# Performance work log

Hardware: AMD Instinct MI355X
Metric: run time of the kernel (lower is better)

## Reference

```python
import jax, jax.numpy as jnp
import numpy as np

B = 32768
Z_DIM = 64
X_DIM = 256
HIDDEN = 512
T = 8            # num_transforms
NBINS = 8
TAIL = 25.0
MULT = 3 * NBINS - 1   # widths + heights + interior derivatives = 23
MIN_W = 1e-3
MIN_H = 1e-3
MIN_D = 1e-3


def _masks():
    # MADE degrees (nflows, random_mask=False)
    d_in = np.arange(1, Z_DIM + 1)                      # input degrees 1..D
    h = np.arange(HIDDEN) % (Z_DIM - 1) + 1             # hidden degrees
    o = np.arange(Z_DIM * MULT) // MULT + 1             # output degrees, MULT contiguous per feature
    m1 = (h[:, None] >= d_in[None, :]).astype(np.float32)   # [H, D]
    m2 = (h[:, None] >= h[None, :]).astype(np.float32)      # [H, H]
    m3 = (o[:, None] > h[None, :]).astype(np.float32)       # [D*MULT, H] strict for output layer
    return jnp.asarray(m1), jnp.asarray(m2), jnp.asarray(m3)


def _rq_spline_fwd(z, uw, uh, ud):
    """Unconstrained rational-quadratic spline with linear tails (forward).
    z: [B, D]; uw/uh: [B, D, NBINS]; ud: [B, D, NBINS-1].
    Returns (outputs [B,D], logabsdet [B,D])."""
    const = np.log(np.exp(1.0 - MIN_D) - 1.0)
    pad = jnp.full(ud.shape[:-1] + (1,), const, ud.dtype)
    ud = jnp.concatenate([pad, ud, pad], axis=-1)       # [B, D, NBINS+1]

    widths = jax.nn.softmax(uw, axis=-1)
    widths = MIN_W + (1.0 - MIN_W * NBINS) * widths
    zero = jnp.zeros(widths.shape[:-1] + (1,), widths.dtype)
    cumw = jnp.concatenate([zero, jnp.cumsum(widths, axis=-1)], axis=-1)
    cumw = -TAIL + 2.0 * TAIL * cumw
    cumw = cumw.at[..., 0].set(-TAIL).at[..., -1].set(TAIL)
    widths = cumw[..., 1:] - cumw[..., :-1]

    derivs = MIN_D + jax.nn.softplus(ud)

    heights = jax.nn.softmax(uh, axis=-1)
    heights = MIN_H + (1.0 - MIN_H * NBINS) * heights
    cumh = jnp.concatenate([zero, jnp.cumsum(heights, axis=-1)], axis=-1)
    cumh = -TAIL + 2.0 * TAIL * cumh
    cumh = cumh.at[..., 0].set(-TAIL).at[..., -1].set(TAIL)
    heights = cumh[..., 1:] - cumh[..., :-1]

    delta = heights / widths

    z_in = jnp.clip(z, -TAIL, TAIL)
    edges = cumw.at[..., -1].add(1e-6)                  # nflows searchsorted eps
    idx = jnp.sum(z_in[..., None] >= edges, axis=-1) - 1
    idx = jnp.clip(idx, 0, NBINS - 1)

    g = lambda a: jnp.take_along_axis(a, idx[..., None], axis=-1)[..., 0]
    in_cw = g(cumw); in_w = g(widths)
    in_ch = g(cumh); in_h = g(heights)
    in_dl = g(delta)
    d0 = g(derivs); d1 = g(derivs[..., 1:])

    th = (z_in - in_cw) / in_w
    th1 = th * (1.0 - th)
    num = in_h * (in_dl * th * th + d0 * th1)
    den = in_dl + (d0 + d1 - 2.0 * in_dl) * th1
    out = in_ch + num / den
    dnum = in_dl ** 2 * (d1 * th * th + 2.0 * in_dl * th1 + d0 * (1.0 - th) ** 2)
    lad = jnp.log(dnum) - 2.0 * jnp.log(den)

    inside = (z >= -TAIL) & (z <= TAIL)
    return jnp.where(inside, out, z), jnp.where(inside, lad, 0.0)


def setup_inputs() -> dict:
    key = jax.random.key(0)
    ks = jax.random.split(key, 10)
    s = 0.05  # small init scale keeps spline params in a sane regime
    return {
        "z": jax.random.normal(ks[0], (B, Z_DIM), jnp.float32),
        "x": jax.random.normal(ks[1], (B, X_DIM), jnp.float32),
        "W1": jax.random.normal(ks[2], (T, HIDDEN, Z_DIM), jnp.float32) * s,
        "b1": jax.random.normal(ks[3], (T, HIDDEN), jnp.float32) * s,
        "Wc": jax.random.normal(ks[4], (T, HIDDEN, X_DIM), jnp.float32) * s,
        "bc": jax.random.normal(ks[5], (T, HIDDEN), jnp.float32) * s,
        "W2": jax.random.normal(ks[6], (T, HIDDEN, HIDDEN), jnp.float32) * s,
        "b2": jax.random.normal(ks[7], (T, HIDDEN), jnp.float32) * s,
        "W3": jax.random.normal(ks[8], (T, Z_DIM * MULT, HIDDEN), jnp.float32) * s,
        "b3": jax.random.normal(ks[9], (T, Z_DIM * MULT), jnp.float32) * s,
    }


def reference(z, x, W1, b1, Wc, bc, W2, b2, W3, b3):
    """log q(z|x) of the composed MADE-RQ-spline flow, shape [B]."""
    m1, m2, m3 = _masks()
    inv_sqrt_h = 1.0 / np.sqrt(HIDDEN)
    cur = z
    total_lad = jnp.zeros(z.shape[0], z.dtype)
    for t in range(T):
        # MADE: masked initial layer + context layer, one masked feedforward block (linear->relu), masked output layer
        h = cur @ (W1[t] * m1).T + b1[t] + x @ Wc[t].T + bc[t]
        h = jax.nn.relu(h @ (W2[t] * m2).T + b2[t])
        p = (h @ (W3[t] * m3).T + b3[t]).reshape(-1, Z_DIM, MULT)
        uw = p[..., :NBINS] * inv_sqrt_h
        uh = p[..., NBINS:2 * NBINS] * inv_sqrt_h
        ud = p[..., 2 * NBINS:]
        cur, lad = _rq_spline_fwd(cur, uw, uh, ud)
        total_lad = total_lad + lad.sum(axis=-1)
    log_base = -0.5 * jnp.sum(cur ** 2, axis=-1) - 0.5 * Z_DIM * np.log(2.0 * np.pi)
    return log_base + total_lad
```

## Files before the change

kernel.cpp:

```cpp
#include <hip/hip_runtime.h>
#include <cstdint>
#include <cstddef>

#define B_ROWS 32768
#define ZD 64
#define XD 256
#define HID 512
#define T_STEPS 8
#define MULT 23
#define MPAD 24
#define NOUT 1472
#define NPAD 1536
#define K1 320
#define PSTRIDE 200

typedef float f32x4 __attribute__((ext_vector_type(4)));
typedef short s16x8 __attribute__((ext_vector_type(8)));

__device__ __forceinline__ unsigned short f2bf(float f) {
  unsigned int u = __float_as_uint(f);
  u = (u + 0x7FFFu + ((u >> 16) & 1u)) >> 16;
  return (unsigned short)u;
}
__device__ __forceinline__ float bf2f(unsigned short s) {
  return __uint_as_float(((unsigned int)s) << 16);
}

__device__ __forceinline__ int permP(int n) {
  return (n < 72) ? (n / 9) + 63 * (n % 9)
                  : ((n - 72) >> 3) + 8 + 63 * ((n - 72) & 7);
}
__device__ __forceinline__ int degP(int n) {
  return (n < 72) ? (n / 9) + 1 : ((n - 72) >> 3) + 9;
}


__global__ void prep_w1cat(const float* __restrict__ W1, const float* __restrict__ Wc,
                           unsigned short* __restrict__ o) {
  int i = blockIdx.x * 256 + threadIdx.x;
  if (i >= T_STEPS * HID * K1) return;
  int t = i / (HID * K1);
  int r = i - t * (HID * K1);
  int n = r / K1;
  int k = r - n * K1;
  int on = permP(n);
  float v;
  if (k < ZD) {
    v = ((on % 63) >= k) ? W1[((size_t)t * HID + on) * ZD + k] : 0.0f;
  } else {
    v = Wc[((size_t)t * HID + on) * XD + (k - ZD)];
  }
  o[i] = f2bf(v);
}

__global__ void prep_w2(const float* __restrict__ W2, unsigned short* __restrict__ o) {
  int i = blockIdx.x * 256 + threadIdx.x;
  if (i >= T_STEPS * HID * HID) return;
  int t = i / (HID * HID);
  int r = i - t * (HID * HID);
  int n = r / HID;
  int k = r - n * HID;
  float v = 0.0f;
  if (degP(n) >= degP(k))
    v = W2[((size_t)t * HID + permP(n)) * HID + permP(k)];
  o[i] = f2bf(v);
}

__global__ void prep_w3(const float* __restrict__ W3, unsigned short* __restrict__ o) {
  int i = blockIdx.x * 256 + threadIdx.x;
  if (i >= T_STEPS * NPAD * HID) return;
  int t = i / (NPAD * HID);
  int r = i - t * (NPAD * HID);
  int n = r / HID;
  int k = r - n * HID;
  int d = n / MPAD;
  int jj = n - d * MPAD;
  float v = 0.0f;
  if (jj < MULT && d >= degP(k))
    v = W3[((size_t)t * NOUT + d * MULT + jj) * HID + permP(k)];
  o[i] = f2bf(v);
}

__global__ void prep_bias(const float* __restrict__ b1, const float* __restrict__ bc,
                          const float* __restrict__ b2, const float* __restrict__ b3,
                          float* __restrict__ ob1, float* __restrict__ ob2,
                          float* __restrict__ ob3) {
  int i = blockIdx.x * 256 + threadIdx.x;
  if (i < T_STEPS * HID) {
    int t = i / HID, n = i - t * HID;
    int on = permP(n);
    ob1[i] = b1[(size_t)t * HID + on] + bc[(size_t)t * HID + on];
  } else if (i < 2 * T_STEPS * HID) {
    int j = i - T_STEPS * HID;
    int t = j / HID, n = j - t * HID;
    ob2[j] = b2[(size_t)t * HID + permP(n)];
  } else {
    int j = i - 2 * T_STEPS * HID;
    if (j < T_STEPS * NPAD) {
      int t = j / NPAD;
      int n = j - t * NPAD;
      int d = n / MPAD;
      int jj = n - d * MPAD;
      ob3[j] = (jj < MULT) ? b3[(size_t)t * NOUT + d * MULT + jj] : 0.0f;
    }
  }
}

__global__ void prep_x(const float* __restrict__ x, unsigned short* __restrict__ A1) {
  int i = blockIdx.x * 256 + threadIdx.x;
  if (i >= B_ROWS * XD) return;
  int b = i >> 8;
  int j = i & 255;
  A1[(size_t)b * K1 + ZD + j] = f2bf(x[i]);
}

__global__ void prep_init(const float* __restrict__ z, unsigned short* __restrict__ A1,
                          float* __restrict__ curf, float* __restrict__ lad) {
  int i = blockIdx.x * 256 + threadIdx.x;
  if (i >= B_ROWS * ZD) return;
  int b = i >> 6;
  int d = i & 63;
  float zv = z[i];
  A1[(size_t)b * K1 + d] = f2bf(zv);
  curf[i] = zv;
  if (d == 0) lad[b] = 0.0f;
}


#define ASYNC16(gp, lp) __builtin_amdgcn_global_load_lds( \
    (__attribute__((address_space(1))) unsigned int*)(gp), \
    (__attribute__((address_space(3))) unsigned int*)(lp), 16, 0, 0)


__global__ __launch_bounds__(256, 2) void gemm_bias(
    const unsigned short* __restrict__ A,
    const unsigned short* __restrict__ Bw,
    const float* __restrict__ bias,
    unsigned short* __restrict__ C,
    int M, int N, int K, int relu, int tri)
{
  __shared__ alignas(16) unsigned short lA[128 * 32];
  __shared__ alignas(16) unsigned short lB[128 * 32];

  const int tid  = threadIdx.x;
  const int lane = tid & 63;
  const int wave = tid >> 6;

  const int lin = blockIdx.y * 4 + blockIdx.x;
  const int xcd = lin & 7;
  const int loc = lin >> 3;
  const int m0 = (xcd * 32 + (loc >> 2)) * 128;
  const int n0 = (loc & 3) * 128;
  const int Keff = tri ? min(K, 192 + n0) : K;

  const int wm = (wave >> 1) * 64;
  const int wn = (wave & 1) * 64;

  const int f    = tid * 16;
  const int row0 = f >> 6;
  const int colb = f & 63;

  char* gA0 = (char*)A  + ((size_t)(m0 + row0) * K) * 2 + colb;
  char* gA1 = gA0 + (size_t)64 * K * 2;
  char* gB0 = (char*)Bw + ((size_t)(n0 + row0) * K) * 2 + colb;
  char* gB1 = gB0 + (size_t)64 * K * 2;

  unsigned short* lA0 = lA + wave * 512;
  unsigned short* lA1 = lA + 2048 + wave * 512;
  unsigned short* lB0 = lB + wave * 512;
  unsigned short* lB1 = lB + 2048 + wave * 512;

  f32x4 acc[4][4];
#pragma unroll
  for (int i = 0; i < 4; i++)
#pragma unroll
    for (int j = 0; j < 4; j++) acc[i][j] = (f32x4){0.f, 0.f, 0.f, 0.f};

  const int fr  = lane & 15;
  const int fkb = (lane >> 4) * 16;
  const char* lab = (const char*)lA;
  const char* lbb = (const char*)lB;

  for (int k0 = 0; k0 < Keff; k0 += 32) {
    ASYNC16(gA0, lA0);
    ASYNC16(gA1, lA1);
    ASYNC16(gB0, lB0);
    ASYNC16(gB1, lB1);
    gA0 += 64; gA1 += 64; gB0 += 64; gB1 += 64;
    __syncthreads();

    s16x8 af[4], bfr[4];
#pragma unroll
    for (int i = 0; i < 4; i++)
      af[i] = *(const s16x8*)(lab + (wm + i * 16 + fr) * 64 + fkb);
#pragma unroll
    for (int i = 0; i < 4; i++)
      bfr[i] = *(const s16x8*)(lbb + (wn + i * 16 + fr) * 64 + fkb);

#pragma unroll
    for (int i = 0; i < 4; i++)
#pragma unroll
      for (int j = 0; j < 4; j++)
        acc[i][j] = __builtin_amdgcn_mfma_f32_16x16x32_bf16(af[i], bfr[j], acc[i][j], 0, 0, 0);
    __syncthreads();
  }

#pragma unroll
  for (int j = 0; j < 4; j++) {
    const int col = n0 + wn + j * 16 + fr;
    const float bv = bias[col];
#pragma unroll
    for (int i = 0; i < 4; i++) {
      const int rbase = m0 + wm + i * 16 + (lane >> 4) * 4;
#pragma unroll
      for (int r = 0; r < 4; r++) {
        float v = acc[i][j][r] + bv;
        if (relu) v = fmaxf(v, 0.0f);
        C[(size_t)(rbase + r) * N + col] = f2bf(v);
      }
    }
  }
}


__device__ __forceinline__ void rq_spline(const unsigned short* __restrict__ pp,
                                          float zv, float& zn, float& lad) {
  const float TAILC = 25.0f;
  const float MIN_WC = 0.001f;
  const float MIN_DC = 0.001f;
  const float SCALE = 0.044194173824159216f;

  s16x8 vw = *(const s16x8*)(pp);
  s16x8 vh = *(const s16x8*)(pp + 8);
  s16x8 vd = *(const s16x8*)(pp + 16);

  bool inside = (zv >= -TAILC) && (zv <= TAILC);
  float z_in = fminf(fmaxf(zv, -TAILC), TAILC);

  float ew[8], eh[8], sw = 0.f, sh = 0.f;
#pragma unroll
  for (int i = 0; i < 8; i++) {
    float u = fminf(fmaxf(bf2f((unsigned short)vw[i]) * SCALE, -30.f), 30.f);
    ew[i] = __expf(u); sw += ew[i];
  }
#pragma unroll
  for (int i = 0; i < 8; i++) {
    float u = fminf(fmaxf(bf2f((unsigned short)vh[i]) * SCALE, -30.f), 30.f);
    eh[i] = __expf(u); sh += eh[i];
  }
  float iw = (1.0f - 8.0f * MIN_WC) / sw;
  float ih = (1.0f - 8.0f * MIN_WC) / sh;

  float cumw[9], cumh[9];
  cumw[0] = -TAILC; cumh[0] = -TAILC;
  float cw = 0.f, ch = 0.f;
#pragma unroll
  for (int i = 0; i < 8; i++) {
    cw += MIN_WC + ew[i] * iw;
    ch += MIN_WC + eh[i] * ih;
    cumw[i + 1] = fmaf(2.0f * TAILC, cw, -TAILC);
    cumh[i + 1] = fmaf(2.0f * TAILC, ch, -TAILC);
  }
  cumw[8] = TAILC; cumh[8] = TAILC;

  int idx = 0;
#pragma unroll
  for (int i = 1; i < 8; i++) idx += (z_in >= cumw[i]) ? 1 : 0;

  float in_cw = 0.f, cw1 = 1.f, in_ch = 0.f, ch1 = 1.f, u0 = 0.f, u1 = 0.f;
#pragma unroll
  for (int i = 0; i < 8; i++) {
    if (i == idx) {
      in_cw = cumw[i]; cw1 = cumw[i + 1];
      in_ch = cumh[i]; ch1 = cumh[i + 1];
      u0 = (i > 0) ? bf2f((unsigned short)vd[i - 1]) : 0.0f;
      u1 = (i < 7) ? bf2f((unsigned short)vd[i]) : 0.0f;
    }
  }
  float dd0 = (idx == 0) ? 1.0f
            : MIN_DC + fmaxf(u0, 0.f) + __logf(1.0f + __expf(-fabsf(u0)));
  float dd1 = (idx == 7) ? 1.0f
            : MIN_DC + fmaxf(u1, 0.f) + __logf(1.0f + __expf(-fabsf(u1)));
  float in_w = cw1 - in_cw;
  float in_h = ch1 - in_ch;

  float delta = in_h / in_w;
  float th  = (z_in - in_cw) / in_w;
  float th1 = th * (1.0f - th);
  float th2 = th * th;
  float num = in_h * (delta * th2 + dd0 * th1);
  float den = delta + (dd0 + dd1 - 2.0f * delta) * th1;
  float outz = in_ch + num / den;
  float omt = 1.0f - th;
  float dnum = delta * delta * (dd1 * th2 + 2.0f * delta * th1 + dd0 * omt * omt);
  float l = __logf(dnum) - 2.0f * __logf(den);

  zn  = inside ? outz : zv;
  lad = inside ? l : 0.0f;
}


__global__ __launch_bounds__(256, 3) void gemm3_spline(
    const unsigned short* __restrict__ A,
    const unsigned short* __restrict__ Bw,
    const float* __restrict__ bias,
    float* __restrict__ curf,
    unsigned short* __restrict__ A1,
    float* __restrict__ lad_acc)
{
  __shared__ alignas(16) union {
    struct { unsigned short A[128 * 32]; unsigned short B[192 * 32]; } g;
    unsigned short p[128 * PSTRIDE];
  } sm;

  const int tid  = threadIdx.x;
  const int lane = tid & 63;
  const int wave = tid >> 6;

  const int lin = blockIdx.y * 8 + blockIdx.x;
  const int xcd = lin & 7;
  const int loc = lin >> 3;
  const int m0 = (xcd * 32 + (loc >> 3)) * 128;
  const int bn = loc & 7;
  const int n0 = bn * 192;
  const int Keff = 64 * (bn + 1);

  const int wm = (wave >> 1) * 64;
  const int wn = (wave & 1) * 96;
  const int fr = lane & 15;

  const int srow = tid >> 1;
  const int sb = m0 + srow;
  const int dl0 = (tid & 1) * 4;
  const int d0 = bn * 8 + dl0;
  float4 cz = *(const float4*)(curf + (size_t)sb * ZD + d0);
  float bv[6];
#pragma unroll
  for (int j = 0; j < 6; j++) bv[j] = bias[n0 + wn + j * 16 + fr];

  const int f    = tid * 16;
  const int row0 = f >> 6;
  const int colb = f & 63;
  const int K = HID;

  char* gA0 = (char*)A  + ((size_t)(m0 + row0) * K) * 2 + colb;
  char* gA1 = gA0 + (size_t)64 * K * 2;
  char* gB0 = (char*)Bw + ((size_t)(n0 + row0) * K) * 2 + colb;
  char* gB1 = gB0 + (size_t)64 * K * 2;
  char* gB2 = gB1 + (size_t)64 * K * 2;

  unsigned short* lA0 = sm.g.A + wave * 512;
  unsigned short* lA1 = sm.g.A + 2048 + wave * 512;
  unsigned short* lB0 = sm.g.B + wave * 512;
  unsigned short* lB1 = sm.g.B + 2048 + wave * 512;
  unsigned short* lB2 = sm.g.B + 4096 + wave * 512;

  f32x4 acc[4][6];
#pragma unroll
  for (int i = 0; i < 4; i++)
#pragma unroll
    for (int j = 0; j < 6; j++) acc[i][j] = (f32x4){0.f, 0.f, 0.f, 0.f};

  const int fkb = (lane >> 4) * 16;
  const char* lab = (const char*)sm.g.A;
  const char* lbb = (const char*)sm.g.B;

  for (int k0 = 0; k0 < Keff; k0 += 32) {
    ASYNC16(gA0, lA0);
    ASYNC16(gA1, lA1);
    ASYNC16(gB0, lB0);
    ASYNC16(gB1, lB1);
    ASYNC16(gB2, lB2);
    gA0 += 64; gA1 += 64; gB0 += 64; gB1 += 64; gB2 += 64;
    __syncthreads();

    s16x8 af[4], bfr[6];
#pragma unroll
    for (int i = 0; i < 4; i++)
      af[i] = *(const s16x8*)(lab + (wm + i * 16 + fr) * 64 + fkb);
#pragma unroll
    for (int j = 0; j < 6; j++)
      bfr[j] = *(const s16x8*)(lbb + (wn + j * 16 + fr) * 64 + fkb);

#pragma unroll
    for (int i = 0; i < 4; i++)
#pragma unroll
      for (int j = 0; j < 6; j++)
        acc[i][j] = __builtin_amdgcn_mfma_f32_16x16x32_bf16(af[i], bfr[j], acc[i][j], 0, 0, 0);
    __syncthreads();
  }

#pragma unroll
  for (int j = 0; j < 6; j++) {
    const int col = wn + j * 16 + fr;
#pragma unroll
    for (int i = 0; i < 4; i++) {
      const int rbase = wm + i * 16 + (lane >> 4) * 4;
#pragma unroll
      for (int r = 0; r < 4; r++)
        sm.p[(rbase + r) * PSTRIDE + col] = f2bf(acc[i][j][r] + bv[j]);
    }
  }
  __syncthreads();

  const unsigned short* pp = sm.p + srow * PSTRIDE + dl0 * MPAD;
  float zn0, zn1, zn2, zn3, l0, l1, l2, l3;
  rq_spline(pp,            cz.x, zn0, l0);
  rq_spline(pp + MPAD,     cz.y, zn1, l1);
  rq_spline(pp + 2 * MPAD, cz.z, zn2, l2);
  rq_spline(pp + 3 * MPAD, cz.w, zn3, l3);

  *(float4*)(curf + (size_t)sb * ZD + d0) = make_float4(zn0, zn1, zn2, zn3);
  union { unsigned int u[2]; unsigned short s[4]; } pk;
  pk.s[0] = f2bf(zn0); pk.s[1] = f2bf(zn1); pk.s[2] = f2bf(zn2); pk.s[3] = f2bf(zn3);
  *(uint2*)(A1 + (size_t)sb * K1 + d0) = make_uint2(pk.u[0], pk.u[1]);

  float s = l0 + l1 + l2 + l3;
  s += __shfl_xor(s, 1, 64);
  if ((tid & 1) == 0) atomicAdd(&lad_acc[sb], s);
}


__global__ void finalize(const float* __restrict__ curf, const float* __restrict__ lad,
                         float* __restrict__ out) {
  int i = blockIdx.x * 256 + threadIdx.x;
  int b = i >> 6;
  int d = i & 63;
  float c = curf[i];
  float q = c * c;
#pragma unroll
  for (int off = 32; off > 0; off >>= 1) q += __shfl_xor(q, off, 64);
  if (d == 0) out[b] = lad[b] - 0.5f * q - 58.81206612509905f;
}


extern "C" void kernel_launch(void* const* d_in, const int* in_sizes, int n_in,
                              void* d_out, int out_size, void* d_ws, size_t ws_size,
                              hipStream_t stream)
{
  const float* z  = (const float*)d_in[0];
  const float* x  = (const float*)d_in[1];
  const float* W1 = (const float*)d_in[2];
  const float* b1 = (const float*)d_in[3];
  const float* Wc = (const float*)d_in[4];
  const float* bc = (const float*)d_in[5];
  const float* W2 = (const float*)d_in[6];
  const float* b2 = (const float*)d_in[7];
  const float* W3 = (const float*)d_in[8];
  const float* b3 = (const float*)d_in[9];
  float* out = (float*)d_out;
  char* ws = (char*)d_ws;

  size_t oA1 = 0;
  size_t oH1 = oA1 + (size_t)B_ROWS * K1 * 2;
  size_t oH2 = oH1 + (size_t)B_ROWS * HID * 2;
  size_t oCU = oH2 + (size_t)B_ROWS * HID * 2;
  size_t oLA = oCU + (size_t)B_ROWS * ZD * 4;
  size_t oW1 = oLA + (size_t)B_ROWS * 4;
  size_t oW2 = oW1 + (size_t)T_STEPS * HID * K1 * 2;
  size_t oW3 = oW2 + (size_t)T_STEPS * HID * HID * 2;
  size_t oB1 = oW3 + (size_t)T_STEPS * NPAD * HID * 2;
  size_t oB2 = oB1 + (size_t)T_STEPS * HID * 4;
  size_t oB3 = oB2 + (size_t)T_STEPS * HID * 4;

  unsigned short* A1  = (unsigned short*)(ws + oA1);
  unsigned short* h1  = (unsigned short*)(ws + oH1);
  unsigned short* h2  = (unsigned short*)(ws + oH2);
  float* curf = (float*)(ws + oCU);
  float* lad  = (float*)(ws + oLA);
  unsigned short* w1c = (unsigned short*)(ws + oW1);
  unsigned short* w2c = (unsigned short*)(ws + oW2);
  unsigned short* w3c = (unsigned short*)(ws + oW3);
  float* b1c = (float*)(ws + oB1);
  float* b2p = (float*)(ws + oB2);
  float* b3c = (float*)(ws + oB3);

  prep_w1cat<<<T_STEPS * HID * K1 / 256, 256, 0, stream>>>(W1, Wc, w1c);
  prep_w2<<<T_STEPS * HID * HID / 256, 256, 0, stream>>>(W2, w2c);
  prep_w3<<<T_STEPS * NPAD * HID / 256, 256, 0, stream>>>(W3, w3c);
  prep_bias<<<T_STEPS * (2 * HID + NPAD) / 256, 256, 0, stream>>>(
      b1, bc, b2, b3, b1c, b2p, b3c);
  prep_x<<<B_ROWS * XD / 256, 256, 0, stream>>>(x, A1);
  prep_init<<<B_ROWS * ZD / 256, 256, 0, stream>>>(z, A1, curf, lad);

  for (int t = 0; t < T_STEPS; ++t) {
    gemm_bias<<<dim3(4, B_ROWS / 128), 256, 0, stream>>>(
        A1, w1c + (size_t)t * HID * K1, b1c + (size_t)t * HID, h1,
        B_ROWS, HID, K1, 0, 0);
    gemm_bias<<<dim3(4, B_ROWS / 128), 256, 0, stream>>>(
        h1, w2c + (size_t)t * HID * HID, b2p + (size_t)t * HID, h2,
        B_ROWS, HID, HID, 1, 1);
    gemm3_spline<<<dim3(8, B_ROWS / 128), 256, 0, stream>>>(
        h2, w3c + (size_t)t * NPAD * HID, b3c + (size_t)t * NPAD,
        curf, A1, lad);
  }
  finalize<<<B_ROWS * ZD / 256, 256, 0, stream>>>(curf, lad, out);
}
```

Before: 998.5 us.

## Load GEMM operands directly from global into registers, bypassing LDS staging

Both GEMM kernels stop staging A/B tiles in shared memory through async global-to-LDS loads and barriers. Each wave now loads its MFMA fragments straight from global memory into registers, and gemm_bias double-buffers them in registers to hide latency. The spline kernel's thread-to-row mapping is changed and its shuffle reduction is replaced by one atomic per thread, and its launch bounds drop to 2 blocks per CU. This removes LDS traffic and syncs, but each wave now reloads shared tiles from L2 without cross-wave reuse, loads become 16-byte strided rows, and register pressure rises.

```diff
diff --git a/kernel.cpp b/kernel.cpp
--- a/kernel.cpp
+++ b/kernel.cpp
@@ -127,11 +127,6 @@
 }
 
 
-#define ASYNC16(gp, lp) __builtin_amdgcn_global_load_lds( \
-    (__attribute__((address_space(1))) unsigned int*)(gp), \
-    (__attribute__((address_space(3))) unsigned int*)(lp), 16, 0, 0)
-
-
 __global__ __launch_bounds__(256, 2) void gemm_bias(
     const unsigned short* __restrict__ A,
     const unsigned short* __restrict__ Bw,
@@ -139,9 +134,6 @@
     unsigned short* __restrict__ C,
     int M, int N, int K, int relu, int tri)
 {
-  __shared__ alignas(16) unsigned short lA[128 * 32];
-  __shared__ alignas(16) unsigned short lB[128 * 32];
-
   const int tid  = threadIdx.x;
   const int lane = tid & 63;
   const int wave = tid >> 6;
@@ -155,20 +147,17 @@
 
   const int wm = (wave >> 1) * 64;
   const int wn = (wave & 1) * 64;
-
-  const int f    = tid * 16;
-  const int row0 = f >> 6;
-  const int colb = f & 63;
-
-  char* gA0 = (char*)A  + ((size_t)(m0 + row0) * K) * 2 + colb;
-  char* gA1 = gA0 + (size_t)64 * K * 2;
-  char* gB0 = (char*)Bw + ((size_t)(n0 + row0) * K) * 2 + colb;
-  char* gB1 = gB0 + (size_t)64 * K * 2;
-
-  unsigned short* lA0 = lA + wave * 512;
-  unsigned short* lA1 = lA + 2048 + wave * 512;
-  unsigned short* lB0 = lB + wave * 512;
-  unsigned short* lB1 = lB + 2048 + wave * 512;
+  const int fr = lane & 15;
+  const int fk = (lane >> 4) * 8;
+
+  const unsigned short* ap[4];
+  const unsigned short* bp[4];
+#pragma unroll
+  for (int i = 0; i < 4; i++)
+    ap[i] = A + (size_t)(m0 + wm + i * 16 + fr) * K + fk;
+#pragma unroll
+  for (int j = 0; j < 4; j++)
+    bp[j] = Bw + (size_t)(n0 + wn + j * 16 + fr) * K + fk;
 
   f32x4 acc[4][4];
 #pragma unroll
@@ -176,34 +165,33 @@
 #pragma unroll
     for (int j = 0; j < 4; j++) acc[i][j] = (f32x4){0.f, 0.f, 0.f, 0.f};
 
-  const int fr  = lane & 15;
-  const int fkb = (lane >> 4) * 16;
-  const char* lab = (const char*)lA;
-  const char* lbb = (const char*)lB;
-
-  for (int k0 = 0; k0 < Keff; k0 += 32) {
-    ASYNC16(gA0, lA0);
-    ASYNC16(gA1, lA1);
-    ASYNC16(gB0, lB0);
-    ASYNC16(gB1, lB1);
-    gA0 += 64; gA1 += 64; gB0 += 64; gB1 += 64;
-    __syncthreads();
-
-    s16x8 af[4], bfr[4];
+  s16x8 a[4], b[4], an[4], bn[4];
+#pragma unroll
+  for (int i = 0; i < 4; i++) a[i] = *(const s16x8*)(ap[i]);
+#pragma unroll
+  for (int j = 0; j < 4; j++) b[j] = *(const s16x8*)(bp[j]);
+
+#pragma unroll 2
+  for (int k0 = 32; k0 < Keff; k0 += 32) {
+#pragma unroll
+    for (int i = 0; i < 4; i++) an[i] = *(const s16x8*)(ap[i] + k0);
+#pragma unroll
+    for (int j = 0; j < 4; j++) bn[j] = *(const s16x8*)(bp[j] + k0);
 #pragma unroll
     for (int i = 0; i < 4; i++)
-      af[i] = *(const s16x8*)(lab + (wm + i * 16 + fr) * 64 + fkb);
-#pragma unroll
-    for (int i = 0; i < 4; i++)
-      bfr[i] = *(const s16x8*)(lbb + (wn + i * 16 + fr) * 64 + fkb);
-
-#pragma unroll
-    for (int i = 0; i < 4; i++)
 #pragma unroll
       for (int j = 0; j < 4; j++)
-        acc[i][j] = __builtin_amdgcn_mfma_f32_16x16x32_bf16(af[i], bfr[j], acc[i][j], 0, 0, 0);
-    __syncthreads();
-  }
+        acc[i][j] = __builtin_amdgcn_mfma_f32_16x16x32_bf16(a[i], b[j], acc[i][j], 0, 0, 0);
+#pragma unroll
+    for (int i = 0; i < 4; i++) a[i] = an[i];
+#pragma unroll
+    for (int j = 0; j < 4; j++) b[j] = bn[j];
+  }
+#pragma unroll
+  for (int i = 0; i < 4; i++)
+#pragma unroll
+    for (int j = 0; j < 4; j++)
+      acc[i][j] = __builtin_amdgcn_mfma_f32_16x16x32_bf16(a[i], b[j], acc[i][j], 0, 0, 0);
 
 #pragma unroll
   for (int j = 0; j < 4; j++) {
@@ -300,7 +288,7 @@
 }
 
 
-__global__ __launch_bounds__(256, 3) void gemm3_spline(
+__global__ __launch_bounds__(256, 2) void gemm3_spline(
     const unsigned short* __restrict__ A,
     const unsigned short* __restrict__ Bw,
     const float* __restrict__ bias,
@@ -308,10 +296,7 @@
     unsigned short* __restrict__ A1,
     float* __restrict__ lad_acc)
 {
-  __shared__ alignas(16) union {
-    struct { unsigned short A[128 * 32]; unsigned short B[192 * 32]; } g;
-    unsigned short p[128 * PSTRIDE];
-  } sm;
+  __shared__ alignas(16) unsigned short pT[128 * PSTRIDE];
 
   const int tid  = threadIdx.x;
   const int lane = tid & 63;
@@ -328,32 +313,25 @@
   const int wm = (wave >> 1) * 64;
   const int wn = (wave & 1) * 96;
   const int fr = lane & 15;
-
-  const int srow = tid >> 1;
+  const int fk = (lane >> 4) * 8;
+
+  const int srow = tid & 127;
   const int sb = m0 + srow;
-  const int dl0 = (tid & 1) * 4;
+  const int dl0 = (tid >> 7) * 4;
   const int d0 = bn * 8 + dl0;
   float4 cz = *(const float4*)(curf + (size_t)sb * ZD + d0);
   float bv[6];
 #pragma unroll
   for (int j = 0; j < 6; j++) bv[j] = bias[n0 + wn + j * 16 + fr];
 
-  const int f    = tid * 16;
-  const int row0 = f >> 6;
-  const int colb = f & 63;
-  const int K = HID;
-
-  char* gA0 = (char*)A  + ((size_t)(m0 + row0) * K) * 2 + colb;
-  char* gA1 = gA0 + (size_t)64 * K * 2;
-  char* gB0 = (char*)Bw + ((size_t)(n0 + row0) * K) * 2 + colb;
-  char* gB1 = gB0 + (size_t)64 * K * 2;
-  char* gB2 = gB1 + (size_t)64 * K * 2;
-
-  unsigned short* lA0 = sm.g.A + wave * 512;
-  unsigned short* lA1 = sm.g.A + 2048 + wave * 512;
-  unsigned short* lB0 = sm.g.B + wave * 512;
-  unsigned short* lB1 = sm.g.B + 2048 + wave * 512;
-  unsigned short* lB2 = sm.g.B + 4096 + wave * 512;
+  const unsigned short* ap[4];
+  const unsigned short* bp[6];
+#pragma unroll
+  for (int i = 0; i < 4; i++)
+    ap[i] = A + (size_t)(m0 + wm + i * 16 + fr) * HID + fk;
+#pragma unroll
+  for (int j = 0; j < 6; j++)
+    bp[j] = Bw + (size_t)(n0 + wn + j * 16 + fr) * HID + fk;
 
   f32x4 acc[4][6];
 #pragma unroll
@@ -361,33 +339,18 @@
 #pragma unroll
     for (int j = 0; j < 6; j++) acc[i][j] = (f32x4){0.f, 0.f, 0.f, 0.f};
 
-  const int fkb = (lane >> 4) * 16;
-  const char* lab = (const char*)sm.g.A;
-  const char* lbb = (const char*)sm.g.B;
-
+#pragma unroll 2
   for (int k0 = 0; k0 < Keff; k0 += 32) {
-    ASYNC16(gA0, lA0);
-    ASYNC16(gA1, lA1);
-    ASYNC16(gB0, lB0);
-    ASYNC16(gB1, lB1);
-    ASYNC16(gB2, lB2);
-    gA0 += 64; gA1 += 64; gB0 += 64; gB1 += 64; gB2 += 64;
-    __syncthreads();
-
-    s16x8 af[4], bfr[6];
+    s16x8 a[4], b[6];
+#pragma unroll
+    for (int i = 0; i < 4; i++) a[i] = *(const s16x8*)(ap[i] + k0);
+#pragma unroll
+    for (int j = 0; j < 6; j++) b[j] = *(const s16x8*)(bp[j] + k0);
 #pragma unroll
     for (int i = 0; i < 4; i++)
-      af[i] = *(const s16x8*)(lab + (wm + i * 16 + fr) * 64 + fkb);
-#pragma unroll
-    for (int j = 0; j < 6; j++)
-      bfr[j] = *(const s16x8*)(lbb + (wn + j * 16 + fr) * 64 + fkb);
-
-#pragma unroll
-    for (int i = 0; i < 4; i++)
 #pragma unroll
       for (int j = 0; j < 6; j++)
-        acc[i][j] = __builtin_amdgcn_mfma_f32_16x16x32_bf16(af[i], bfr[j], acc[i][j], 0, 0, 0);
-    __syncthreads();
+        acc[i][j] = __builtin_amdgcn_mfma_f32_16x16x32_bf16(a[i], b[j], acc[i][j], 0, 0, 0);
   }
 
 #pragma unroll
@@ -398,12 +361,12 @@
       const int rbase = wm + i * 16 + (lane >> 4) * 4;
 #pragma unroll
       for (int r = 0; r < 4; r++)
-        sm.p[(rbase + r) * PSTRIDE + col] = f2bf(acc[i][j][r] + bv[j]);
+        pT[(rbase + r) * PSTRIDE + col] = f2bf(acc[i][j][r] + bv[j]);
     }
   }
   __syncthreads();
 
-  const unsigned short* pp = sm.p + srow * PSTRIDE + dl0 * MPAD;
+  const unsigned short* pp = pT + srow * PSTRIDE + dl0 * MPAD;
   float zn0, zn1, zn2, zn3, l0, l1, l2, l3;
   rq_spline(pp,            cz.x, zn0, l0);
   rq_spline(pp + MPAD,     cz.y, zn1, l1);
@@ -415,9 +378,7 @@
   pk.s[0] = f2bf(zn0); pk.s[1] = f2bf(zn1); pk.s[2] = f2bf(zn2); pk.s[3] = f2bf(zn3);
   *(uint2*)(A1 + (size_t)sb * K1 + d0) = make_uint2(pk.u[0], pk.u[1]);
 
-  float s = l0 + l1 + l2 + l3;
-  s += __shfl_xor(s, 1, 64);
-  if ((tid & 1) == 0) atomicAdd(&lad_acc[sb], s);
+  atomicAdd(&lad_acc[sb], l0 + l1 + l2 + l3);
 }
 
 
```

After: 2.142 ms. +114.5%, slower.
